# Optimization experiments

Hardware: AMD Instinct MI355X
Metric: run time of the kernel (lower is better)

## Reference

```python
import jax, jax.numpy as jnp
import numpy as np

DIM = 320
HEADS = 8
D_HEAD = 40
CTX_DIM = 768
INNER_FF = 4 * DIM  # 1280
EPS = 1e-5


def _ln(x, w, b):
    mu = jnp.mean(x, axis=-1, keepdims=True)
    var = jnp.mean(jnp.square(x - mu), axis=-1, keepdims=True)
    return (x - mu) * jax.lax.rsqrt(var + EPS) * w + b


def _attn(xq, ctx, Wq, Wk, Wv, Wo, bo):
    # Wq: [dim, inner]; Wk/Wv: [ctx_dim, inner]; Wo: [inner, dim]
    b, n, _ = xq.shape
    m = ctx.shape[1]
    scale = D_HEAD ** -0.5
    q = (xq @ Wq).reshape(b, n, HEADS, D_HEAD)
    k = (ctx @ Wk).reshape(b, m, HEADS, D_HEAD)
    v = (ctx @ Wv).reshape(b, m, HEADS, D_HEAD)
    sim = jnp.einsum('bihd,bjhd->bhij', q, k) * scale
    attn = jax.nn.softmax(sim, axis=-1)
    out = jnp.einsum('bhij,bjhd->bihd', attn, v).reshape(b, n, HEADS * D_HEAD)
    return out @ Wo + bo


def setup_inputs() -> dict:
    key = jax.random.key(0)
    ks = jax.random.split(key, 20)
    s = 0.02
    inner = HEADS * D_HEAD  # 320
    d = {
        'x': jax.random.normal(ks[0], (2, 4096, DIM), jnp.float32),
        'context': jax.random.normal(ks[1], (2, 77, CTX_DIM), jnp.float32),
        # norm params
        'ln1_w': jnp.ones((DIM,)), 'ln1_b': jnp.zeros((DIM,)),
        'ln2_w': jnp.ones((DIM,)), 'ln2_b': jnp.zeros((DIM,)),
        'ln3_w': jnp.ones((DIM,)), 'ln3_b': jnp.zeros((DIM,)),
        # attn1 (self)
        'a1_Wq': jax.random.normal(ks[2], (DIM, inner)) * s,
        'a1_Wk': jax.random.normal(ks[3], (DIM, inner)) * s,
        'a1_Wv': jax.random.normal(ks[4], (DIM, inner)) * s,
        'a1_Wo': jax.random.normal(ks[5], (inner, DIM)) * s,
        'a1_bo': jnp.zeros((DIM,)),
        # attn2 (cross)
        'a2_Wq': jax.random.normal(ks[6], (DIM, inner)) * s,
        'a2_Wk': jax.random.normal(ks[7], (CTX_DIM, inner)) * s,
        'a2_Wv': jax.random.normal(ks[8], (CTX_DIM, inner)) * s,
        'a2_Wo': jax.random.normal(ks[9], (inner, DIM)) * s,
        'a2_bo': jnp.zeros((DIM,)),
        # GEGLU feed-forward
        'ff_W1': jax.random.normal(ks[10], (DIM, 2 * INNER_FF)) * s,
        'ff_b1': jnp.zeros((2 * INNER_FF,)),
        'ff_W2': jax.random.normal(ks[11], (INNER_FF, DIM)) * s,
        'ff_b2': jnp.zeros((DIM,)),
    }
    return d


def reference(x, context, ln1_w, ln1_b, ln2_w, ln2_b, ln3_w, ln3_b,
              a1_Wq, a1_Wk, a1_Wv, a1_Wo, a1_bo,
              a2_Wq, a2_Wk, a2_Wv, a2_Wo, a2_bo,
              ff_W1, ff_b1, ff_W2, ff_b2):
    h = _ln(x, ln1_w, ln1_b)
    x = _attn(h, h, a1_Wq, a1_Wk, a1_Wv, a1_Wo, a1_bo) + x
    h = _ln(x, ln2_w, ln2_b)
    x = _attn(h, context, a2_Wq, a2_Wk, a2_Wv, a2_Wo, a2_bo) + x
    h = _ln(x, ln3_w, ln3_b)
    proj = h @ ff_W1 + ff_b1
    u, gate = jnp.split(proj, 2, axis=-1)
    ff = (u * jax.nn.gelu(gate, approximate=False)) @ ff_W2 + ff_b2
    return ff + x
```

## Files before the change

kernel.cpp:

```cpp
#include <hip/hip_runtime.h>
#include <hip/hip_bf16.h>
#include <math.h>

typedef __hip_bfloat16 bf16;
typedef __attribute__((ext_vector_type(8))) short bf16x8;
typedef __attribute__((ext_vector_type(4))) short bf16x4;
typedef __attribute__((ext_vector_type(4))) float f32x4;
typedef __attribute__((ext_vector_type(2))) unsigned int u32x2;

#define DIM 320
#define HEADS 8
#define DHEAD 40
#define CTXD 768
#define FFI 1280
#define NQ 4096
#define NCTX 77
#define BATCH 2

static __device__ __forceinline__ short f2bs(float v) {
    union { bf16 b; short s; } x; x.b = __float2bfloat16(v); return x.s;
}
static __device__ __forceinline__ unsigned pkbf(float hi, float lo) {
    return __builtin_amdgcn_perm(__float_as_uint(hi), __float_as_uint(lo), 0x07060302u);
}

__global__ void __launch_bounds__(256) wtrans_all(
    const float* q1s, const float* k1s, const float* v1s, const float* o1s,
    const float* q2s, const float* o2s, const float* k2s, const float* v2s,
    const float* w1s, const float* w2s,
    short* q1d, short* k1d, short* v1d, short* o1d,
    short* q2d, short* o2d, short* k2d, short* v2d,
    short* w1d, short* w2d)
{
    int bid = blockIdx.x;
    const float* W; short* Wt; int K, N, base;
    if (bid < 600) {
        int ws = bid / 100; base = bid % 100; K = DIM; N = DIM;
        W  = ws == 0 ? q1s : ws == 1 ? k1s : ws == 2 ? v1s : ws == 3 ? o1s : ws == 4 ? q2s : o2s;
        Wt = ws == 0 ? q1d : ws == 1 ? k1d : ws == 2 ? v1d : ws == 3 ? o1d : ws == 4 ? q2d : o2d;
    } else if (bid < 1080) {
        int i = bid - 600; int ws = i / 240; base = i % 240; K = CTXD; N = DIM;
        W = ws ? v2s : k2s; Wt = ws ? v2d : k2d;
    } else if (bid < 1880) {
        base = bid - 1080; K = DIM; N = 2 * FFI; W = w1s; Wt = w1d;
    } else {
        base = bid - 1880; K = FFI; N = DIM; W = w2s; Wt = w2d;
    }
    int ntx = N / 32;
    int n0 = (base % ntx) * 32, k0 = (base / ntx) * 32;
    __shared__ float T[32][33];
    int c = threadIdx.x & 31, r8 = threadIdx.x >> 5;
#pragma unroll
    for (int rr = 0; rr < 4; ++rr) {
        int r = r8 + rr * 8;
        T[r][c] = W[(size_t)(k0 + r) * N + n0 + c];
    }
    __syncthreads();
#pragma unroll
    for (int rr = 0; rr < 4; ++rr) {
        int r = r8 + rr * 8;
        Wt[(size_t)(n0 + r) * K + k0 + c] = f2bs(T[c][r]);
    }
}

__global__ void __launch_bounds__(256) ln_kernel(const float* __restrict__ src,
                          const float* __restrict__ w, const float* __restrict__ bp,
                          short* __restrict__ out, int rows)
{
    int row = blockIdx.x * 4 + (threadIdx.x >> 6);
    int lane = threadIdx.x & 63;
    if (row >= rows) return;
    float v[5];
    float s = 0.f, s2 = 0.f;
#pragma unroll
    for (int t = 0; t < 5; ++t) {
        int c = lane + t * 64;
        float x = src[(size_t)row * DIM + c];
        v[t] = x; s += x; s2 += x * x;
    }
#pragma unroll
    for (int off = 32; off; off >>= 1) { s += __shfl_xor(s, off); s2 += __shfl_xor(s2, off); }
    float mean = s * (1.f / DIM);
    float var = s2 * (1.f / DIM) - mean * mean;
    float rstd = rsqrtf(var + 1e-5f);
#pragma unroll
    for (int t = 0; t < 5; ++t) {
        int c = lane + t * 64;
        out[(size_t)row * DIM + c] = f2bs((v[t] - mean) * rstd * w[c] + bp[c]);
    }
}


template<int MODE>
__global__ void __launch_bounds__(256) gemm128(const short* __restrict__ A,
                          const short* __restrict__ Wt,
                          const float* __restrict__ bias,
                          const float* __restrict__ res,
                          float* __restrict__ xbuf,
                          short* __restrict__ outb,
                          float* __restrict__ outf,
                          int N, int K, float oscale)
{
    __shared__ short As[128 * 72];
    __shared__ short Bs[64 * 72];
    const int tid = threadIdx.x;
    const int w = tid >> 6, lane = tid & 63, lrow = lane & 15, lgrp = lane >> 4;
    const int wr = w >> 1, wc = w & 1;
    const int m0 = blockIdx.y * 128, n0 = blockIdx.x * 64;
    f32x4 acc[4][2] = {};
    for (int k0 = 0; k0 < K; k0 += 64) {
        __syncthreads();
#pragma unroll
        for (int l = 0; l < 4; ++l) {
            int idx = tid + (l << 8);
            int arow = idx >> 3, ac = idx & 7;
            *(bf16x8*)&As[arow * 72 + ac * 8] =
                *(const bf16x8*)(A + (size_t)(m0 + arow) * K + k0 + ac * 8);
        }
#pragma unroll
        for (int l = 0; l < 2; ++l) {
            int idx = tid + (l << 8);
            int brow = idx >> 3, bc = idx & 7;
            *(bf16x8*)&Bs[brow * 72 + bc * 8] =
                *(const bf16x8*)(Wt + (size_t)(n0 + brow) * K + k0 + bc * 8);
        }
        __syncthreads();
#pragma unroll
        for (int s = 0; s < 2; ++s) {
            bf16x8 b0 = *(const bf16x8*)&Bs[(wc * 32 + lrow) * 72 + s * 32 + lgrp * 8];
            bf16x8 b1 = *(const bf16x8*)&Bs[(wc * 32 + 16 + lrow) * 72 + s * 32 + lgrp * 8];
#pragma unroll
            for (int m = 0; m < 4; ++m) {
                bf16x8 a = *(const bf16x8*)&As[(wr * 64 + m * 16 + lrow) * 72 + s * 32 + lgrp * 8];
                acc[m][0] = __builtin_amdgcn_mfma_f32_16x16x32_bf16(a, b0, acc[m][0], 0, 0, 0);
                acc[m][1] = __builtin_amdgcn_mfma_f32_16x16x32_bf16(a, b1, acc[m][1], 0, 0, 0);
            }
        }
    }
#pragma unroll
    for (int n = 0; n < 2; ++n) {
        int col = n0 + wc * 32 + n * 16 + lrow;
        float bvx = bias ? bias[col] : 0.f;
#pragma unroll
        for (int m = 0; m < 4; ++m) {
#pragma unroll
            for (int r = 0; r < 4; ++r) {
                int row = m0 + wr * 64 + m * 16 + lgrp * 4 + r;
                float v = acc[m][n][r] + bvx;
                size_t o = (size_t)row * N + col;
                if (MODE == 0)      outb[o] = f2bs(v * oscale);
                else if (MODE == 1) xbuf[o] = v + res[o];
                else if (MODE == 2) xbuf[o] += v;
                else                outf[o] = v + xbuf[o];
            }
        }
    }
}

__global__ void __launch_bounds__(256) qkv128(const short* __restrict__ A,
                          const short* __restrict__ wq, const short* __restrict__ wk,
                          const short* __restrict__ wv,
                          short* __restrict__ qb, short* __restrict__ kbuf,
                          short* __restrict__ vts, float qscale)
{
    __shared__ short As[128 * 72];
    __shared__ short Bs[64 * 72];
    const int tid = threadIdx.x;
    const int z = blockIdx.z;
    const short* Wt = z == 0 ? wq : z == 1 ? wk : wv;
    const int w = tid >> 6, lane = tid & 63, lrow = lane & 15, lgrp = lane >> 4;
    const int wr = w >> 1, wc = w & 1;
    const int m0 = blockIdx.y * 128, n0 = blockIdx.x * 64;
    f32x4 acc[4][2] = {};
    for (int k0 = 0; k0 < DIM; k0 += 64) {
        __syncthreads();
#pragma unroll
        for (int l = 0; l < 4; ++l) {
            int idx = tid + (l << 8);
            int arow = idx >> 3, ac = idx & 7;
            *(bf16x8*)&As[arow * 72 + ac * 8] =
                *(const bf16x8*)(A + (size_t)(m0 + arow) * DIM + k0 + ac * 8);
        }
#pragma unroll
        for (int l = 0; l < 2; ++l) {
            int idx = tid + (l << 8);
            int brow = idx >> 3, bc = idx & 7;
            *(bf16x8*)&Bs[brow * 72 + bc * 8] =
                *(const bf16x8*)(Wt + (size_t)(n0 + brow) * DIM + k0 + bc * 8);
        }
        __syncthreads();
#pragma unroll
        for (int s = 0; s < 2; ++s) {
            bf16x8 b0 = *(const bf16x8*)&Bs[(wc * 32 + lrow) * 72 + s * 32 + lgrp * 8];
            bf16x8 b1 = *(const bf16x8*)&Bs[(wc * 32 + 16 + lrow) * 72 + s * 32 + lgrp * 8];
#pragma unroll
            for (int m = 0; m < 4; ++m) {
                bf16x8 a = *(const bf16x8*)&As[(wr * 64 + m * 16 + lrow) * 72 + s * 32 + lgrp * 8];
                acc[m][0] = __builtin_amdgcn_mfma_f32_16x16x32_bf16(a, b0, acc[m][0], 0, 0, 0);
                acc[m][1] = __builtin_amdgcn_mfma_f32_16x16x32_bf16(a, b1, acc[m][1], 0, 0, 0);
            }
        }
    }
#pragma unroll
    for (int n = 0; n < 2; ++n) {
        int col = n0 + wc * 32 + n * 16 + lrow;
#pragma unroll
        for (int m = 0; m < 4; ++m) {
            if (z == 2) {
                int row0 = m0 + wr * 64 + m * 16 + lgrp * 4;
                int b_ = row0 >> 12, kv = row0 & (NQ - 1);
                int hh = col / DHEAD, d = col - hh * DHEAD;
                bf16x4 pv;
#pragma unroll
                for (int r = 0; r < 4; ++r) pv[r] = f2bs(acc[m][n][r]);
                *(bf16x4*)(vts + (size_t)((b_ * HEADS + hh) * 48 + d) * NQ + kv) = pv;
            } else {
#pragma unroll
                for (int r = 0; r < 4; ++r) {
                    int row = m0 + wr * 64 + m * 16 + lgrp * 4 + r;
                    float v = acc[m][n][r];
                    if (z == 0) qb[(size_t)row * DIM + col] = f2bs(v * qscale);
                    else        kbuf[(size_t)row * DIM + col] = f2bs(v);
                }
            }
        }
    }
}

__global__ void __launch_bounds__(256) geglu128(const short* __restrict__ A,
                           const short* __restrict__ Wt1,
                           const float* __restrict__ b1, short* __restrict__ G)
{
    __shared__ short As[128 * 72];
    __shared__ short Bu[64 * 72];
    __shared__ short Bg[64 * 72];
    const int tid = threadIdx.x;
    const int w = tid >> 6, lane = tid & 63, lrow = lane & 15, lgrp = lane >> 4;
    const int wr = w >> 1, wc = w & 1;
    const int m0 = blockIdx.y * 128, n0 = blockIdx.x * 64;
    f32x4 au[4][2] = {}, ag[4][2] = {};
    for (int k0 = 0; k0 < DIM; k0 += 64) {
        __syncthreads();
#pragma unroll
        for (int l = 0; l < 4; ++l) {
            int idx = tid + (l << 8);
            int arow = idx >> 3, ac = idx & 7;
            *(bf16x8*)&As[arow * 72 + ac * 8] =
                *(const bf16x8*)(A + (size_t)(m0 + arow) * DIM + k0 + ac * 8);
        }
#pragma unroll
        for (int l = 0; l < 2; ++l) {
            int idx = tid + (l << 8);
            int brow = idx >> 3, bc = idx & 7;
            *(bf16x8*)&Bu[brow * 72 + bc * 8] =
                *(const bf16x8*)(Wt1 + (size_t)(n0 + brow) * DIM + k0 + bc * 8);
            *(bf16x8*)&Bg[brow * 72 + bc * 8] =
                *(const bf16x8*)(Wt1 + (size_t)(FFI + n0 + brow) * DIM + k0 + bc * 8);
        }
        __syncthreads();
#pragma unroll
        for (int s = 0; s < 2; ++s) {
            bf16x8 bu0 = *(const bf16x8*)&Bu[(wc * 32 + lrow) * 72 + s * 32 + lgrp * 8];
            bf16x8 bu1 = *(const bf16x8*)&Bu[(wc * 32 + 16 + lrow) * 72 + s * 32 + lgrp * 8];
            bf16x8 bg0 = *(const bf16x8*)&Bg[(wc * 32 + lrow) * 72 + s * 32 + lgrp * 8];
            bf16x8 bg1 = *(const bf16x8*)&Bg[(wc * 32 + 16 + lrow) * 72 + s * 32 + lgrp * 8];
#pragma unroll
            for (int m = 0; m < 4; ++m) {
                bf16x8 a = *(const bf16x8*)&As[(wr * 64 + m * 16 + lrow) * 72 + s * 32 + lgrp * 8];
                au[m][0] = __builtin_amdgcn_mfma_f32_16x16x32_bf16(a, bu0, au[m][0], 0, 0, 0);
                au[m][1] = __builtin_amdgcn_mfma_f32_16x16x32_bf16(a, bu1, au[m][1], 0, 0, 0);
                ag[m][0] = __builtin_amdgcn_mfma_f32_16x16x32_bf16(a, bg0, ag[m][0], 0, 0, 0);
                ag[m][1] = __builtin_amdgcn_mfma_f32_16x16x32_bf16(a, bg1, ag[m][1], 0, 0, 0);
            }
        }
    }
#pragma unroll
    for (int n = 0; n < 2; ++n) {
        int col = n0 + wc * 32 + n * 16 + lrow;
        float bu = b1[col], bg = b1[FFI + col];
#pragma unroll
        for (int m = 0; m < 4; ++m) {
#pragma unroll
            for (int r = 0; r < 4; ++r) {
                int row = m0 + wr * 64 + m * 16 + lgrp * 4 + r;
                float u = au[m][n][r] + bu;
                float g = ag[m][n][r] + bg;
                float gelu = 0.5f * g * (1.f + erff(g * 0.70710678f));
                G[(size_t)row * FFI + col] = f2bs(u * gelu);
            }
        }
    }
}

__global__ void __launch_bounds__(256) mfma_crosskv(const float* __restrict__ ctx,
                          const short* __restrict__ wk2, const short* __restrict__ wv2,
                          short* __restrict__ k2, short* __restrict__ vt2)
{
    __shared__ short As[64 * 72];
    __shared__ short Bs[64 * 72];
    const int tid = threadIdx.x;
    const int z = blockIdx.z;
    const short* Wt = z ? wv2 : wk2;
    const int Mc = BATCH * NCTX;
    const int w = tid >> 6, lane = tid & 63, lrow = lane & 15, lgrp = lane >> 4;
    const int m0 = blockIdx.y * 64, n0 = blockIdx.x * 64;
    f32x4 acc[4] = {};
    for (int kb = 0; kb < CTXD / 64; ++kb) {
        const int k0 = kb << 6;
        __syncthreads();
#pragma unroll
        for (int l = 0; l < 2; ++l) {
            int idx = tid + (l << 8);
            int arow = idx >> 3, ac = idx & 7;
            int grow = m0 + arow;
            bf16x8 v = {};
            if (grow < Mc) {
                const float* Af = ctx + (size_t)grow * CTXD + k0 + ac * 8;
#pragma unroll
                for (int j = 0; j < 8; ++j) v[j] = f2bs(Af[j]);
            }
            *(bf16x8*)&As[arow * 72 + ac * 8] = v;
            *(bf16x8*)&Bs[arow * 72 + ac * 8] =
                *(const bf16x8*)(Wt + (size_t)(n0 + arow) * CTXD + k0 + ac * 8);
        }
        __syncthreads();
#pragma unroll
        for (int s = 0; s < 2; ++s) {
            bf16x8 a = *(const bf16x8*)&As[(w * 16 + lrow) * 72 + s * 32 + lgrp * 8];
#pragma unroll
            for (int ct = 0; ct < 4; ++ct) {
                bf16x8 b = *(const bf16x8*)&Bs[(ct * 16 + lrow) * 72 + s * 32 + lgrp * 8];
                acc[ct] = __builtin_amdgcn_mfma_f32_16x16x32_bf16(a, b, acc[ct], 0, 0, 0);
            }
        }
    }
#pragma unroll
    for (int ct = 0; ct < 4; ++ct) {
        int col = n0 + ct * 16 + lrow;
#pragma unroll
        for (int r = 0; r < 4; ++r) {
            int row = m0 + w * 16 + lgrp * 4 + r;
            if (row >= Mc) continue;
            float v = acc[ct][r];
            if (z == 0) k2[(size_t)row * DIM + col] = f2bs(v);
            else {
                int b_ = row / NCTX, kv = row - b_ * NCTX;
                int hh = col / DHEAD, d = col - hh * DHEAD;
                vt2[(size_t)((b_ * HEADS + hh) * 48 + d) * 128 + kv] = f2bs(v);
            }
        }
    }
}

template<bool FULL>
__global__ void __launch_bounds__(512) flash_mfma(const short* __restrict__ Q,
                           const short* __restrict__ Kb,
                           const short* __restrict__ VtG,
                           short* __restrict__ O,
                           int kvlen, int kvs)
{
    __shared__ short Ks[2][64 * 64];
    __shared__ short Vt[2][48 * 64];
    __shared__ short Ps[128 * 64];
    const int tid = threadIdx.x;
    const int w = tid >> 6, lane = tid & 63, lrow = lane & 15, lgrp = lane >> 4;
    const int hh = blockIdx.y, b = blockIdx.z;
    const int q0 = blockIdx.x * 128;
    const int swz = (lrow & 7) << 4;

    if (tid < 512) { ((bf16x8*)Ks[0])[tid] = (bf16x8){}; ((bf16x8*)Ks[1])[tid] = (bf16x8){}; }
    if (tid < 384) {
        short fill = ((tid >> 3) == 40) ? (short)0x3F80 : (short)0;
        bf16x8 f8 = {fill, fill, fill, fill, fill, fill, fill, fill};
        ((bf16x8*)Vt[0])[tid] = f8; ((bf16x8*)Vt[1])[tid] = f8;
    }

    const size_t qbase = ((size_t)(b * NQ + q0 + w * 16 + lrow)) * DIM + hh * DHEAD;
    bf16x8 bq0 = *(const bf16x8*)(Q + qbase + lgrp * 8);
    bf16x8 bq1 = {};
    if (lgrp == 0) bq1 = *(const bf16x8*)(Q + qbase + 32);

    const bool isK = tid < 320;
    const int kv0 = isK ? tid / 5 : 0, cc0 = isK ? tid % 5 : 0;
    const int vc0 = tid - 320;
    const int vd0 = vc0 >> 3, vcc0 = vc0 & 7;
    const bool hasV1 = tid < 192;
    const int vd1 = (192 + tid) >> 3, vcc1 = (192 + tid) & 7;
    const bool wrV1 = hasV1 && (vd1 < DHEAD);

    bf16x8 st0, st1;
    const size_t kbase = (size_t)b * kvlen;
    const size_t vbase = (size_t)((b * HEADS + hh) * 48);

    auto issue = [&](int t) {
        const int j0 = t << 6;
        st0 = (bf16x8){};
        if (isK) {
            if (FULL || j0 + kv0 < kvlen)
                st0 = *(const bf16x8*)(Kb + (kbase + j0 + kv0) * DIM + hh * DHEAD + cc0 * 8);
        } else {
            st0 = *(const bf16x8*)(VtG + (vbase + vd0) * kvs + j0 + vcc0 * 8);
            if (!FULL && j0 + 63 >= kvlen) {
#pragma unroll
                for (int j = 0; j < 8; ++j) if (j0 + vcc0 * 8 + j >= kvlen) st0[j] = 0;
            }
        }
        if (wrV1) {
            st1 = *(const bf16x8*)(VtG + (vbase + vd1) * kvs + j0 + vcc1 * 8);
            if (!FULL && j0 + 63 >= kvlen) {
#pragma unroll
                for (int j = 0; j < 8; ++j) if (j0 + vcc1 * 8 + j >= kvlen) st1[j] = 0;
            }
        }
    };
    auto commit = [&](int bi) {
        if (isK)
            *(bf16x8*)((char*)Ks[bi] + kv0 * 128 + ((cc0 * 16) ^ ((kv0 & 7) << 4))) = st0;
        else
            *(bf16x8*)((char*)Vt[bi] + vd0 * 128 + ((vcc0 * 16) ^ ((vd0 & 7) << 4))) = st0;
        if (wrV1)
            *(bf16x8*)((char*)Vt[bi] + vd1 * 128 + ((vcc1 * 16) ^ ((vd1 & 7) << 4))) = st1;
    };

    f32x4 o_acc[3] = {};

    issue(0);
    __syncthreads();
    commit(0);
    const int ntiles = (kvlen + 63) >> 6;
    char* prow = (char*)Ps + (w * 16 + lrow) * 128;
    for (int t = 0; t < ntiles; ++t) {
        const int j0 = t << 6;
        const int bi = t & 1;
        __syncthreads();
        if (t + 1 < ntiles) issue(t + 1);

        f32x4 sacc[4] = {};
        __builtin_amdgcn_s_setprio(1);
#pragma unroll
        for (int ct = 0; ct < 4; ++ct) {
            const char* krow = (char*)Ks[bi] + (ct * 16 + lrow) * 128;
            bf16x8 ak0 = *(const bf16x8*)(krow + ((lgrp * 16) ^ swz));
            sacc[ct] = __builtin_amdgcn_mfma_f32_16x16x32_bf16(ak0, bq0, sacc[ct], 0, 0, 0);
            bf16x8 ak1 = *(const bf16x8*)(krow + ((64 + lgrp * 16) ^ swz));
            sacc[ct] = __builtin_amdgcn_mfma_f32_16x16x32_bf16(ak1, bq1, sacc[ct], 0, 0, 0);
        }
        __builtin_amdgcn_s_setprio(0);
        if (!FULL && j0 + 64 > kvlen) {
#pragma unroll
            for (int ct = 0; ct < 4; ++ct)
#pragma unroll
                for (int r = 0; r < 4; ++r)
                    if (j0 + ct * 16 + lgrp * 4 + r >= kvlen) sacc[ct][r] = -1e30f;
        }
#pragma unroll
        for (int ct = 0; ct < 4; ++ct) {
            float p0 = __builtin_amdgcn_exp2f(sacc[ct][0]);
            float p1 = __builtin_amdgcn_exp2f(sacc[ct][1]);
            float p2 = __builtin_amdgcn_exp2f(sacc[ct][2]);
            float p3 = __builtin_amdgcn_exp2f(sacc[ct][3]);
            u32x2 pk; pk[0] = pkbf(p1, p0); pk[1] = pkbf(p3, p2);
            *(u32x2*)(prow + ((ct * 32 + lgrp * 8) ^ swz)) = pk;
        }
        __builtin_amdgcn_s_setprio(1);
#pragma unroll
        for (int s = 0; s < 2; ++s) {
            bf16x8 bp = *(const bf16x8*)(prow + ((s * 64 + lgrp * 16) ^ swz));
#pragma unroll
            for (int dt = 0; dt < 3; ++dt) {
                bf16x8 av = *(const bf16x8*)((char*)Vt[bi] + (dt * 16 + lrow) * 128 + ((s * 64 + lgrp * 16) ^ swz));
                o_acc[dt] = __builtin_amdgcn_mfma_f32_16x16x32_bf16(av, bp, o_acc[dt], 0, 0, 0);
            }
        }
        __builtin_amdgcn_s_setprio(0);
        if (t + 1 < ntiles) commit((t + 1) & 1);
    }
    float lsum = __shfl(o_acc[2][0], 32 + (lane & 15));
    float invl = 1.f / lsum;
    const size_t obase = ((size_t)(b * NQ + q0 + w * 16 + lrow)) * DIM + hh * DHEAD;
#pragma unroll
    for (int dt = 0; dt < 3; ++dt) {
        int dbase = dt * 16 + lgrp * 4;
        if (dbase < DHEAD) {
            u32x2 ov;
            ov[0] = pkbf(o_acc[dt][1] * invl, o_acc[dt][0] * invl);
            ov[1] = pkbf(o_acc[dt][3] * invl, o_acc[dt][2] * invl);
            *(u32x2*)(O + obase + dbase) = ov;
        }
    }
}

extern "C" void kernel_launch(void* const* d_in, const int* in_sizes, int n_in,
                              void* d_out, int out_size, void* d_ws, size_t ws_size,
                              hipStream_t stream)
{
    const float* x      = (const float*)d_in[0];
    const float* ctx    = (const float*)d_in[1];
    const float* ln1_w  = (const float*)d_in[2];
    const float* ln1_b  = (const float*)d_in[3];
    const float* ln2_w  = (const float*)d_in[4];
    const float* ln2_b  = (const float*)d_in[5];
    const float* ln3_w  = (const float*)d_in[6];
    const float* ln3_b  = (const float*)d_in[7];
    const float* a1_Wq  = (const float*)d_in[8];
    const float* a1_Wk  = (const float*)d_in[9];
    const float* a1_Wv  = (const float*)d_in[10];
    const float* a1_Wo  = (const float*)d_in[11];
    const float* a1_bo  = (const float*)d_in[12];
    const float* a2_Wq  = (const float*)d_in[13];
    const float* a2_Wk  = (const float*)d_in[14];
    const float* a2_Wv  = (const float*)d_in[15];
    const float* a2_Wo  = (const float*)d_in[16];
    const float* a2_bo  = (const float*)d_in[17];
    const float* ff_W1  = (const float*)d_in[18];
    const float* ff_b1  = (const float*)d_in[19];
    const float* ff_W2  = (const float*)d_in[20];
    const float* ff_b2  = (const float*)d_in[21];

    const int M = BATCH * NQ;
    const float qscale2 = (float)(0.15811388300841898 * 1.4426950408889634);

    char* p = (char*)d_ws;
    auto carve = [&](size_t bytes) { char* r = p; p += (bytes + 255) & ~255ULL; return r; };
    short* h       = (short*)carve((size_t)M * DIM * 2);
    short* qb      = (short*)carve((size_t)M * DIM * 2);
    short* kbuf    = (short*)carve((size_t)M * DIM * 2);
    short* attnout = (short*)carve((size_t)M * DIM * 2);
    float* xbuf    = (float*)carve((size_t)M * DIM * 4);
    short* gbuf    = (short*)carve((size_t)M * FFI * 2);
    short* VtS     = (short*)carve((size_t)BATCH * HEADS * 48 * NQ * 2);
    short* Vt2     = (short*)carve((size_t)BATCH * HEADS * 48 * 128 * 2);
    short* k2      = (short*)carve((size_t)256 * DIM * 2);
    short* wtq1    = (short*)carve((size_t)DIM * DIM * 2);
    short* wtk1    = (short*)carve((size_t)DIM * DIM * 2);
    short* wtv1    = (short*)carve((size_t)DIM * DIM * 2);
    short* wto1    = (short*)carve((size_t)DIM * DIM * 2);
    short* wtq2    = (short*)carve((size_t)DIM * DIM * 2);
    short* wto2    = (short*)carve((size_t)DIM * DIM * 2);
    short* wtk2    = (short*)carve((size_t)DIM * CTXD * 2);
    short* wtv2    = (short*)carve((size_t)DIM * CTXD * 2);
    short* wt1     = (short*)carve((size_t)2 * FFI * DIM * 2);
    short* wt2     = (short*)carve((size_t)DIM * FFI * 2);

    dim3 blk(256);
    dim3 g128(DIM / 64, M / 128);
    dim3 gattn(NQ / 128, HEADS, BATCH);

    wtrans_all<<<2280, blk, 0, stream>>>(a1_Wq, a1_Wk, a1_Wv, a1_Wo, a2_Wq, a2_Wo,
                                         a2_Wk, a2_Wv, ff_W1, ff_W2,
                                         wtq1, wtk1, wtv1, wto1, wtq2, wto2,
                                         wtk2, wtv2, wt1, wt2);
    ln_kernel<<<M / 4, blk, 0, stream>>>(x, ln1_w, ln1_b, h, M);
    qkv128<<<dim3(5, 64, 3), blk, 0, stream>>>(h, wtq1, wtk1, wtv1, qb, kbuf, VtS, qscale2);
    flash_mfma<true><<<gattn, dim3(512), 0, stream>>>(qb, kbuf, VtS, attnout, NQ, NQ);
    gemm128<1><<<g128, blk, 0, stream>>>(attnout, wto1, a1_bo, x, xbuf, nullptr, nullptr, DIM, DIM, 1.f);
    ln_kernel<<<M / 4, blk, 0, stream>>>(xbuf, ln2_w, ln2_b, h, M);
    gemm128<0><<<g128, blk, 0, stream>>>(h, wtq2, nullptr, nullptr, nullptr, qb, nullptr, DIM, DIM, qscale2);
    mfma_crosskv<<<dim3(5, 3, 2), blk, 0, stream>>>(ctx, wtk2, wtv2, k2, Vt2);
    flash_mfma<false><<<gattn, dim3(512), 0, stream>>>(qb, k2, Vt2, attnout, NCTX, 128);
    gemm128<2><<<g128, blk, 0, stream>>>(attnout, wto2, a2_bo, nullptr, xbuf, nullptr, nullptr, DIM, DIM, 1.f);
    ln_kernel<<<M / 4, blk, 0, stream>>>(xbuf, ln3_w, ln3_b, h, M);
    geglu128<<<dim3(FFI / 64, M / 128), blk, 0, stream>>>(h, wt1, ff_b1, gbuf);
    gemm128<3><<<g128, blk, 0, stream>>>(gbuf, wt2, ff_b2, nullptr, xbuf, nullptr, (float*)d_out, DIM, FFI, 1.f);
}
```

Measured before the change: 239.5 us.

## Store residual stream in bf16, vectorize layernorm, drop KV tail masking

The fp32 residual buffer becomes a bf16 buffer, which halves residual traffic in the output-projection GEMM epilogues and the layernorm reads. Layernorm now uses 40 lanes that each load and store 8 contiguous elements. The attention loader no longer zero-masks K/V loads past kvlen and issues the next tile's loads before the barrier. Risks are lower residual precision accumulated across stages and possible out-of-range or garbage K/V reads in the cross-attention tail, which relies on score masking and padded buffers.

```diff
diff --git a/kernel.cpp b/kernel.cpp
--- a/kernel.cpp
+++ b/kernel.cpp
@@ -19,6 +19,9 @@
 
 static __device__ __forceinline__ short f2bs(float v) {
     union { bf16 b; short s; } x; x.b = __float2bfloat16(v); return x.s;
+}
+static __device__ __forceinline__ float bs2f(short s) {
+    return __uint_as_float(((unsigned)(unsigned short)s) << 16);
 }
 static __device__ __forceinline__ unsigned pkbf(float hi, float lo) {
     return __builtin_amdgcn_perm(__float_as_uint(hi), __float_as_uint(lo), 0x07060302u);
@@ -63,40 +66,46 @@
     }
 }
 
-__global__ void __launch_bounds__(256) ln_kernel(const float* __restrict__ src,
+template<bool SRCB16>
+__global__ void __launch_bounds__(256) ln_kernel(const void* __restrict__ srcp,
                           const float* __restrict__ w, const float* __restrict__ bp,
                           short* __restrict__ out, int rows)
 {
     int row = blockIdx.x * 4 + (threadIdx.x >> 6);
     int lane = threadIdx.x & 63;
-    if (row >= rows) return;
-    float v[5];
+    float v[8];
     float s = 0.f, s2 = 0.f;
-#pragma unroll
-    for (int t = 0; t < 5; ++t) {
-        int c = lane + t * 64;
-        float x = src[(size_t)row * DIM + c];
-        v[t] = x; s += x; s2 += x * x;
+    if (lane < 40) {
+        if (SRCB16) {
+            bf16x8 xv = *(const bf16x8*)((const short*)srcp + (size_t)row * DIM + lane * 8);
+#pragma unroll
+            for (int j = 0; j < 8; ++j) { v[j] = bs2f(xv[j]); s += v[j]; s2 += v[j] * v[j]; }
+        } else {
+            const float* rp = (const float*)srcp + (size_t)row * DIM + lane * 8;
+#pragma unroll
+            for (int j = 0; j < 8; ++j) { v[j] = rp[j]; s += v[j]; s2 += v[j] * v[j]; }
+        }
     }
 #pragma unroll
     for (int off = 32; off; off >>= 1) { s += __shfl_xor(s, off); s2 += __shfl_xor(s2, off); }
     float mean = s * (1.f / DIM);
     float var = s2 * (1.f / DIM) - mean * mean;
     float rstd = rsqrtf(var + 1e-5f);
-#pragma unroll
-    for (int t = 0; t < 5; ++t) {
-        int c = lane + t * 64;
-        out[(size_t)row * DIM + c] = f2bs((v[t] - mean) * rstd * w[c] + bp[c]);
-    }
-}
-
+    if (lane < 40) {
+        bf16x8 ov;
+#pragma unroll
+        for (int j = 0; j < 8; ++j)
+            ov[j] = f2bs((v[j] - mean) * rstd * w[lane * 8 + j] + bp[lane * 8 + j]);
+        *(bf16x8*)(out + (size_t)row * DIM + lane * 8) = ov;
+    }
+}
 
 template<int MODE>
 __global__ void __launch_bounds__(256) gemm128(const short* __restrict__ A,
                           const short* __restrict__ Wt,
                           const float* __restrict__ bias,
                           const float* __restrict__ res,
-                          float* __restrict__ xbuf,
+                          short* __restrict__ resb,
                           short* __restrict__ outb,
                           float* __restrict__ outf,
                           int N, int K, float oscale)
@@ -149,9 +158,9 @@
                 float v = acc[m][n][r] + bvx;
                 size_t o = (size_t)row * N + col;
                 if (MODE == 0)      outb[o] = f2bs(v * oscale);
-                else if (MODE == 1) xbuf[o] = v + res[o];
-                else if (MODE == 2) xbuf[o] += v;
-                else                outf[o] = v + xbuf[o];
+                else if (MODE == 1) resb[o] = f2bs(v + res[o]);
+                else if (MODE == 2) resb[o] = f2bs(v + bs2f(resb[o]));
+                else                outf[o] = v + bs2f(resb[o]);
             }
         }
     }
@@ -394,24 +403,12 @@
 
     auto issue = [&](int t) {
         const int j0 = t << 6;
-        st0 = (bf16x8){};
-        if (isK) {
-            if (FULL || j0 + kv0 < kvlen)
-                st0 = *(const bf16x8*)(Kb + (kbase + j0 + kv0) * DIM + hh * DHEAD + cc0 * 8);
-        } else {
+        if (isK)
+            st0 = *(const bf16x8*)(Kb + (kbase + j0 + kv0) * DIM + hh * DHEAD + cc0 * 8);
+        else
             st0 = *(const bf16x8*)(VtG + (vbase + vd0) * kvs + j0 + vcc0 * 8);
-            if (!FULL && j0 + 63 >= kvlen) {
-#pragma unroll
-                for (int j = 0; j < 8; ++j) if (j0 + vcc0 * 8 + j >= kvlen) st0[j] = 0;
-            }
-        }
-        if (wrV1) {
+        if (wrV1)
             st1 = *(const bf16x8*)(VtG + (vbase + vd1) * kvs + j0 + vcc1 * 8);
-            if (!FULL && j0 + 63 >= kvlen) {
-#pragma unroll
-                for (int j = 0; j < 8; ++j) if (j0 + vcc1 * 8 + j >= kvlen) st1[j] = 0;
-            }
-        }
     };
     auto commit = [&](int bi) {
         if (isK)
@@ -432,8 +429,8 @@
     for (int t = 0; t < ntiles; ++t) {
         const int j0 = t << 6;
         const int bi = t & 1;
-        __syncthreads();
         if (t + 1 < ntiles) issue(t + 1);
+        __syncthreads();
 
         f32x4 sacc[4] = {};
         __builtin_amdgcn_s_setprio(1);
@@ -526,7 +523,7 @@
     short* qb      = (short*)carve((size_t)M * DIM * 2);
     short* kbuf    = (short*)carve((size_t)M * DIM * 2);
     short* attnout = (short*)carve((size_t)M * DIM * 2);
-    float* xbuf    = (float*)carve((size_t)M * DIM * 4);
+    short* resb    = (short*)carve((size_t)M * DIM * 2);
     short* gbuf    = (short*)carve((size_t)M * FFI * 2);
     short* VtS     = (short*)carve((size_t)BATCH * HEADS * 48 * NQ * 2);
     short* Vt2     = (short*)carve((size_t)BATCH * HEADS * 48 * 128 * 2);
@@ -550,16 +547,16 @@
                                          a2_Wk, a2_Wv, ff_W1, ff_W2,
                                          wtq1, wtk1, wtv1, wto1, wtq2, wto2,
                                          wtk2, wtv2, wt1, wt2);
-    ln_kernel<<<M / 4, blk, 0, stream>>>(x, ln1_w, ln1_b, h, M);
+    ln_kernel<false><<<M / 4, blk, 0, stream>>>(x, ln1_w, ln1_b, h, M);
     qkv128<<<dim3(5, 64, 3), blk, 0, stream>>>(h, wtq1, wtk1, wtv1, qb, kbuf, VtS, qscale2);
     flash_mfma<true><<<gattn, dim3(512), 0, stream>>>(qb, kbuf, VtS, attnout, NQ, NQ);
-    gemm128<1><<<g128, blk, 0, stream>>>(attnout, wto1, a1_bo, x, xbuf, nullptr, nullptr, DIM, DIM, 1.f);
-    ln_kernel<<<M / 4, blk, 0, stream>>>(xbuf, ln2_w, ln2_b, h, M);
+    gemm128<1><<<g128, blk, 0, stream>>>(attnout, wto1, a1_bo, x, resb, nullptr, nullptr, DIM, DIM, 1.f);
+    ln_kernel<true><<<M / 4, blk, 0, stream>>>(resb, ln2_w, ln2_b, h, M);
     gemm128<0><<<g128, blk, 0, stream>>>(h, wtq2, nullptr, nullptr, nullptr, qb, nullptr, DIM, DIM, qscale2);
     mfma_crosskv<<<dim3(5, 3, 2), blk, 0, stream>>>(ctx, wtk2, wtv2, k2, Vt2);
     flash_mfma<false><<<gattn, dim3(512), 0, stream>>>(qb, k2, Vt2, attnout, NCTX, 128);
-    gemm128<2><<<g128, blk, 0, stream>>>(attnout, wto2, a2_bo, nullptr, xbuf, nullptr, nullptr, DIM, DIM, 1.f);
-    ln_kernel<<<M / 4, blk, 0, stream>>>(xbuf, ln3_w, ln3_b, h, M);
+    gemm128<2><<<g128, blk, 0, stream>>>(attnout, wto2, a2_bo, nullptr, resb, nullptr, nullptr, DIM, DIM, 1.f);
+    ln_kernel<true><<<M / 4, blk, 0, stream>>>(resb, ln3_w, ln3_b, h, M);
     geglu128<<<dim3(FFI / 64, M / 128), blk, 0, stream>>>(h, wt1, ff_b1, gbuf);
-    gemm128<3><<<g128, blk, 0, stream>>>(gbuf, wt2, ff_b2, nullptr, xbuf, nullptr, (float*)d_out, DIM, FFI, 1.f);
-}
+    gemm128<3><<<g128, blk, 0, stream>>>(gbuf, wt2, ff_b2, nullptr, resb, nullptr, (float*)d_out, DIM, FFI, 1.f);
+}
```

After: 236.2 us. No clear change (-1.4%).
